# Kernel optimization log

Measured on AMD Instinct MI355X. Metric: run time of the kernel, lower is better.

The kernel has to match this reference:

```python
import jax, jax.numpy as jnp
import numpy as np

B, S, D, E, N, K = 4, 2048, 1024, 2048, 16, 4

def setup_inputs() -> dict:
    key = jax.random.key(0)
    ks = jax.random.split(key, 16)
    w = lambda k, shape, s=0.02: jax.random.normal(k, shape, dtype=jnp.float32) * s
    return {
        "x": jax.random.normal(ks[0], (B, S, D), dtype=jnp.float32),
        "ln_g": jnp.ones((D,), jnp.float32),
        "ln_b": jnp.zeros((D,), jnp.float32),
        "W_in": w(ks[1], (2 * E, D)),
        "b_in": jnp.zeros((2 * E,), jnp.float32),
        "conv_w": w(ks[2], (E, 1, K), 0.1),
        "conv_b": jnp.zeros((E,), jnp.float32),
        "A": w(ks[3], (E, N), 0.1),
        "Bm": w(ks[4], (E, N), 0.1),
        "W_c": w(ks[5], (E, E)),
        "b_c": jnp.zeros((E,), jnp.float32),
        "W_d": w(ks[6], (E, E)),
        "b_d": jnp.zeros((E,), jnp.float32),
        "log_delta": jnp.zeros((E,), jnp.float32),
        "W_out": w(ks[7], (D, E)),
        "b_out": jnp.zeros((D,), jnp.float32),
    }

def _layernorm(x, g, b, eps=1e-5):
    mu = jnp.mean(x, axis=-1, keepdims=True)
    var = jnp.var(x, axis=-1, keepdims=True)
    return (x - mu) * jax.lax.rsqrt(var + eps) * g + b

def _forward(x, ln_g, ln_b, W_in, b_in, conv_w, conv_b, A, Bm, W_c, b_c, W_d, b_d, log_delta, W_out, b_out):
    x_ln = _layernorm(x, ln_g, ln_b)
    x_proj = jnp.einsum("bsd,ed->bse", x_ln, W_in) + b_in  # (B,S,2E)
    xp, gate = jnp.split(x_proj, 2, axis=-1)
    # causal depthwise conv1d (torch pads K-1 both sides then truncates -> left pad only)
    xc = jax.lax.conv_general_dilated(
        xp.transpose(0, 2, 1), conv_w, (1,), [(K - 1, 0)],
        dimension_numbers=("NCH", "OIH", "NCH"), feature_group_count=E)
    xc = (xc + conv_b[None, :, None]).transpose(0, 2, 1)  # (B,S,E)
    xc = jax.nn.silu(xc)
    # selective SSM
    delta = jax.nn.softplus(log_delta)
    A_diag = jnp.exp(-delta)  # (E,)
    u = (jnp.einsum("bse,fe->bsf", xc, W_c) + b_c) * jax.nn.sigmoid(jnp.einsum("bse,fe->bsf", xc, W_d) + b_d)
    def step(h, u_t):
        # h: (B,E,N), u_t: (B,E)
        h = h * A_diag[None, :, None] + u_t[:, :, None] * Bm[None]
        y = jnp.sum(h * A[None], axis=-1)  # (B,E)
        return h, y
    h0 = jnp.zeros((x.shape[0], E, N), x.dtype)
    _, ys = jax.lax.scan(step, h0, u.transpose(1, 0, 2))  # ys: (S,B,E)
    x_ssm = ys.transpose(1, 0, 2)
    x_gated = x_ssm * jax.nn.sigmoid(gate)
    out = jnp.einsum("bse,de->bsd", x_gated, W_out) + b_out
    return out + x

def reference(x, ln_g, ln_b, W_in, b_in, conv_w, conv_b, A, Bm, W_c, b_c, W_d, b_d, log_delta, W_out, b_out):
    return _forward(x, ln_g, ln_b, W_in, b_in, conv_w, conv_b, A, Bm, W_c, b_c, W_d, b_d, log_delta, W_out, b_out)
```

## Files before the change

### kernel.cpp

```cpp
#include <hip/hip_runtime.h>
#include <hip/hip_bf16.h>

typedef __bf16 bf16_t;
typedef unsigned char u8;
typedef __bf16 bf16x8 __attribute__((ext_vector_type(8)));
typedef __bf16 bf16x4 __attribute__((ext_vector_type(4)));
typedef float  f32x4  __attribute__((ext_vector_type(4)));
typedef int    i32x4  __attribute__((ext_vector_type(4)));
typedef int    i32x8  __attribute__((ext_vector_type(8)));
typedef __attribute__((address_space(3))) unsigned as3u32;
typedef __attribute__((address_space(1))) unsigned as1u32;

#define Bdim 4
#define Sdim 2048
#define Ddim 1024
#define Edim 2048
#define CH 64
#define CL 32

#define WSCALE 32.0f
#define XCSCALE 16.0f
#define GSCALE 256.0f

__device__ __forceinline__ void gload_lds16(const void* g, void* l) {
  __builtin_amdgcn_global_load_lds((const as1u32*)g, (as3u32*)l, 16, 0, 0);
}
__device__ __forceinline__ float sigmoidf_(float x) {
  return 1.f / (1.f + __expf(-x));
}
__device__ __forceinline__ int pk_fp8x4(float a, float b, float c, float d) {
  int p = __builtin_amdgcn_cvt_pk_fp8_f32(a, b, 0, 0);
  p = __builtin_amdgcn_cvt_pk_fp8_f32(c, d, p, 1);
  return p;
}

__global__ __launch_bounds__(256)
void cvt_fp8_3(const float* __restrict__ s0, const float* __restrict__ s1,
               const float* __restrict__ s2, u8* __restrict__ d0,
               u8* __restrict__ d1, u8* __restrict__ d2) {
  const int seg = blockIdx.x >> 12;
  const int i   = ((blockIdx.x & 4095) * 256 + threadIdx.x) * 4;
  const float* s = (seg == 0) ? s0 : (seg == 1) ? s1 : s2;
  u8*          d = (seg == 0) ? d0 : (seg == 1) ? d1 : d2;
  *(int*)(d + i) = pk_fp8x4(s[i] * WSCALE, s[i + 1] * WSCALE,
                            s[i + 2] * WSCALE, s[i + 3] * WSCALE);
}

__global__ __launch_bounds__(256)
void cvt_fp8(const float* __restrict__ s, u8* __restrict__ d, int n, float scale) {
  int i = (blockIdx.x * 256 + threadIdx.x) * 4;
  if (i < n)
    *(int*)(d + i) = pk_fp8x4(s[i] * scale, s[i + 1] * scale,
                              s[i + 2] * scale, s[i + 3] * scale);
}

__global__ __launch_bounds__(256)
void prep_scalars(const float* __restrict__ ld, const float* __restrict__ Am,
                  const float* __restrict__ Bm, float* __restrict__ aexp,
                  float* __restrict__ Ce) {
  int e = blockIdx.x * 256 + threadIdx.x;
  if (e >= Edim) return;
  float d = ld[e];
  float sp = (d > 20.f) ? d : log1pf(expf(d));
  aexp[e] = expf(-sp);
  float s = 0.f;
  #pragma unroll
  for (int n = 0; n < 16; ++n) s += Am[e * 16 + n] * Bm[e * 16 + n];
  Ce[e] = s;
}

__global__ __launch_bounds__(256)
void ln_kernel(const float* __restrict__ x, const float* __restrict__ g,
               const float* __restrict__ b, u8* __restrict__ out) {
  const int row = blockIdx.x;
  const int tid = threadIdx.x;
  const float4 v = ((const float4*)(x + (size_t)row * Ddim))[tid];
  float s  = v.x + v.y + v.z + v.w;
  float ss = v.x * v.x + v.y * v.y + v.z * v.z + v.w * v.w;
  #pragma unroll
  for (int o = 32; o > 0; o >>= 1) { s += __shfl_down(s, o); ss += __shfl_down(ss, o); }
  __shared__ float sh[8];
  const int wv = tid >> 6, lane = tid & 63;
  if (lane == 0) { sh[wv] = s; sh[4 + wv] = ss; }
  __syncthreads();
  s  = sh[0] + sh[1] + sh[2] + sh[3];
  ss = sh[4] + sh[5] + sh[6] + sh[7];
  const float mean = s * (1.f / Ddim);
  const float var  = ss * (1.f / Ddim) - mean * mean;
  const float rstd = rsqrtf(var + 1e-5f);
  const float4 gv = ((const float4*)g)[tid];
  const float4 bv = ((const float4*)b)[tid];
  *(int*)(out + (size_t)row * Ddim + tid * 4) =
      pk_fp8x4((v.x - mean) * rstd * gv.x + bv.x,
               (v.y - mean) * rstd * gv.y + bv.y,
               (v.z - mean) * rstd * gv.z + bv.z,
               (v.w - mean) * rstd * gv.w + bv.w);
}

#define BM 128
#define BN 128

template<int MODE>
__global__ __launch_bounds__(256)
void gemm_mx(const u8* __restrict__ A, const u8* __restrict__ Bw,
             const float* __restrict__ bias, const bf16_t* __restrict__ X,
             const float* __restrict__ R, bf16_t* __restrict__ Cb,
             float* __restrict__ Cf, float descale, int M, int N, int K) {
  __shared__ __align__(16) u8 As[BM * 128];
  __shared__ __align__(16) u8 Bs[BN * 128];

  const int tid  = threadIdx.x;
  const int lane = tid & 63;
  const int wv   = tid >> 6;
  const int m0   = blockIdx.y * BM;
  const int n0   = blockIdx.x * BN;

  const int wr = (wv >> 1) * 64;
  const int wc = (wv & 1) * 64;
  const int tq = lane >> 4;
  const int tr = lane & 15;

  f32x4 acc[4][4] = {};

  size_t srcOff[4];
  int    ldsOff[4];
  #pragma unroll
  for (int g = 0; g < 4; ++g) {
    const int p   = g * 256 + tid;
    const int row = p >> 3;
    const int c   = (p & 7) ^ (row & 7);
    srcOff[g] = (size_t)row * K + c * 16;
    ldsOff[g] = g * 4096 + wv * 1024;
  }
  const size_t aBase = (size_t)m0 * K;
  const size_t bBase = (size_t)n0 * K;
  char* AsB = (char*)As;
  char* BsB = (char*)Bs;

  const int s7 = tr & 7;
  const int p0 = (((tq << 1)) ^ s7) * 16;
  const int p1 = (((tq << 1) | 1) ^ s7) * 16;

  for (int k0 = 0; k0 < K; k0 += 128) {
    __syncthreads();
    #pragma unroll
    for (int g = 0; g < 4; ++g)
      gload_lds16(A + aBase + srcOff[g] + k0, AsB + ldsOff[g]);
    #pragma unroll
    for (int g = 0; g < 4; ++g)
      gload_lds16(Bw + bBase + srcOff[g] + k0, BsB + ldsOff[g]);
    __syncthreads();

    i32x8 aF[4], bF[4];
    #pragma unroll
    for (int i = 0; i < 4; ++i) {
      const int rb = (wr + i * 16 + tr) * 128;
      const i32x4 lo = *(const i32x4*)&As[rb + p0];
      const i32x4 hi = *(const i32x4*)&As[rb + p1];
      aF[i] = __builtin_shufflevector(lo, hi, 0, 1, 2, 3, 4, 5, 6, 7);
    }
    #pragma unroll
    for (int j = 0; j < 4; ++j) {
      const int rb = (wc + j * 16 + tr) * 128;
      const i32x4 lo = *(const i32x4*)&Bs[rb + p0];
      const i32x4 hi = *(const i32x4*)&Bs[rb + p1];
      bF[j] = __builtin_shufflevector(lo, hi, 0, 1, 2, 3, 4, 5, 6, 7);
    }
    #pragma unroll
    for (int i = 0; i < 4; ++i)
      #pragma unroll
      for (int j = 0; j < 4; ++j)
        acc[i][j] = __builtin_amdgcn_mfma_scale_f32_16x16x128_f8f6f4(
            aF[i], bF[j], acc[i][j], 0, 0, 0, 0x7F, 0, 0x7F);
  }

  #pragma unroll
  for (int i = 0; i < 4; ++i) {
    #pragma unroll
    for (int j = 0; j < 4; ++j) {
      const int col = n0 + wc + j * 16 + tr;
      const float bv = bias[col];
      #pragma unroll
      for (int r = 0; r < 4; ++r) {
        const int rowg = m0 + wr + i * 16 + tq * 4 + r;
        const size_t idx = (size_t)rowg * N + col;
        const float v = acc[i][j][r] * descale + bv;
        if (MODE == 1)      Cf[idx] = v + R[idx];
        else if (MODE == 2) Cb[idx] = (bf16_t)((float)X[idx] * sigmoidf_(v));
        else                Cb[idx] = (bf16_t)v;
      }
    }
  }
}

__global__ __launch_bounds__(256)
void conv_silu(const bf16_t* __restrict__ xpg, const float* __restrict__ cw,
               const float* __restrict__ cb, u8* __restrict__ xc) {
  const int e  = blockIdx.y * 256 + threadIdx.x;
  const int b  = blockIdx.x >> 9;
  const int s0 = (blockIdx.x & 511) * 4;
  const float w0 = cw[e * 4 + 0], w1 = cw[e * 4 + 1], w2 = cw[e * 4 + 2], w3 = cw[e * 4 + 3];
  const float bias = cb[e];
  float xv[7];
  #pragma unroll
  for (int j = 0; j < 7; ++j) {
    const int s = s0 - 3 + j;
    xv[j] = (s >= 0) ? (float)xpg[(size_t)(b * Sdim + s) * (2 * Edim) + e] : 0.f;
  }
  #pragma unroll
  for (int t = 0; t < 4; ++t) {
    float a = fmaf(w0, xv[t], fmaf(w1, xv[t + 1], fmaf(w2, xv[t + 2], fmaf(w3, xv[t + 3], bias))));
    float y = a * sigmoidf_(a) * XCSCALE;
    int p = __builtin_amdgcn_cvt_pk_fp8_f32(y, y, 0, 0);
    xc[(size_t)(b * Sdim + s0 + t) * Edim + e] = (u8)(p & 0xff);
  }
}

__global__ __launch_bounds__(256)
void scan_part1(const bf16_t* __restrict__ u, const float* __restrict__ aexp,
                float* __restrict__ zloc) {
  const int c    = blockIdx.x;
  const int b    = blockIdx.y >> 3;
  const int eblk = blockIdx.y & 7;
  const int e    = eblk * 256 + threadIdx.x;
  const float a  = aexp[e];
  const bf16_t* up = u + ((size_t)(b * Sdim + c * CL)) * Edim + e;
  float z = 0.f;
  #pragma unroll
  for (int t = 0; t < CL; ++t) z = fmaf(a, z, (float)up[(size_t)t * Edim]);
  zloc[((size_t)b * CH + c) * Edim + e] = z;
}

__global__ __launch_bounds__(256)
void scan_part2(const float* __restrict__ aexp, float* __restrict__ zloc) {
  const int idx = blockIdx.x * 256 + threadIdx.x;
  const int b = idx >> 11, e = idx & (Edim - 1);
  float a  = aexp[e];
  float aL = a * a;
  aL = aL * aL; aL = aL * aL; aL = aL * aL; aL = aL * aL;
  float* zp = zloc + (size_t)b * CH * Edim + e;
  float pref = 0.f;
  #pragma unroll 4
  for (int c = 0; c < CH; ++c) {
    const float loc = zp[(size_t)c * Edim];
    zp[(size_t)c * Edim] = pref;
    pref = fmaf(aL, pref, loc);
  }
}

__global__ __launch_bounds__(256)
void scan_part3(const bf16_t* __restrict__ u, const bf16_t* __restrict__ xpg,
                const float* __restrict__ aexp, const float* __restrict__ Ce,
                const float* __restrict__ zloc, u8* __restrict__ xg8) {
  const int c    = blockIdx.x;
  const int b    = blockIdx.y >> 3;
  const int eblk = blockIdx.y & 7;
  const int e    = eblk * 256 + threadIdx.x;
  const float a = aexp[e], C = Ce[e];
  float z = zloc[((size_t)b * CH + c) * Edim + e];
  const bf16_t* up = u   + ((size_t)(b * Sdim + c * CL)) * Edim + e;
  const bf16_t* gp = xpg + ((size_t)(b * Sdim + c * CL)) * (2 * Edim) + Edim + e;
  u8*           op = xg8 + ((size_t)(b * Sdim + c * CL)) * Edim + e;
  #pragma unroll 8
  for (int t = 0; t < CL; ++t) {
    z = fmaf(a, z, (float)up[(size_t)t * Edim]);
    const float gv = (float)gp[(size_t)t * (2 * Edim)];
    const float y  = C * z * sigmoidf_(gv) * GSCALE;
    int p = __builtin_amdgcn_cvt_pk_fp8_f32(y, y, 0, 0);
    op[(size_t)t * Edim] = (u8)(p & 0xff);
  }
}

extern "C" void kernel_launch(void* const* d_in, const int* in_sizes, int n_in,
                              void* d_out, int out_size, void* d_ws, size_t ws_size,
                              hipStream_t stream) {
  const float* x         = (const float*)d_in[0];
  const float* ln_g      = (const float*)d_in[1];
  const float* ln_b      = (const float*)d_in[2];
  const float* W_in      = (const float*)d_in[3];
  const float* b_in      = (const float*)d_in[4];
  const float* conv_w    = (const float*)d_in[5];
  const float* conv_b    = (const float*)d_in[6];
  const float* Am        = (const float*)d_in[7];
  const float* Bm        = (const float*)d_in[8];
  const float* W_c       = (const float*)d_in[9];
  const float* b_c       = (const float*)d_in[10];
  const float* W_d       = (const float*)d_in[11];
  const float* b_d       = (const float*)d_in[12];
  const float* log_delta = (const float*)d_in[13];
  const float* W_out     = (const float*)d_in[14];
  const float* b_out     = (const float*)d_in[15];
  float* out = (float*)d_out;

  const size_t MiB = 1024 * 1024;
  char* w = (char*)d_ws;
  u8*     wWin8  = (u8*)    (w + 0);
  u8*     wWc8   = (u8*)    (w + 4 * MiB);
  u8*     wWd8   = (u8*)    (w + 8 * MiB);
  u8*     wWout8 = (u8*)    (w + 12 * MiB);
  float*  aexp   = (float*) (w + 15 * MiB);
  float*  Ce     = (float*) (w + 15 * MiB + 16384);
  float*  zloc   = (float*) (w + 15 * MiB + 65536);
  u8*     xln8   = (u8*)    (w + 18 * MiB);
  bf16_t* xpg    = (bf16_t*)(w + 26 * MiB);
  u8*     xc8    = (u8*)    (w + 90 * MiB);
  bf16_t* cbuf   = (bf16_t*)(w + 106 * MiB);
  bf16_t* ubuf   = (bf16_t*)(w + 138 * MiB);
  u8*     xg8    = (u8*)    (w + 170 * MiB);

  const int M = Bdim * Sdim;
  const float dsIn  = 1.f / WSCALE;
  const float dsCD  = 1.f / (WSCALE * XCSCALE);
  const float dsOut = 1.f / (WSCALE * GSCALE);

  cvt_fp8_3<<<3 * 4096, 256, 0, stream>>>(W_in, W_c, W_d, wWin8, wWc8, wWd8);
  cvt_fp8<<<(Ddim * Edim) / 1024, 256, 0, stream>>>(W_out, wWout8, Ddim * Edim, WSCALE);
  prep_scalars<<<Edim / 256, 256, 0, stream>>>(log_delta, Am, Bm, aexp, Ce);

  ln_kernel<<<M, 256, 0, stream>>>(x, ln_g, ln_b, xln8);

  gemm_mx<0><<<dim3((2 * Edim) / BN, M / BM), 256, 0, stream>>>(
      xln8, wWin8, b_in, nullptr, nullptr, xpg, nullptr, dsIn, M, 2 * Edim, Ddim);

  conv_silu<<<dim3(Bdim * (Sdim / 4), Edim / 256), 256, 0, stream>>>(xpg, conv_w, conv_b, xc8);

  gemm_mx<0><<<dim3(Edim / BN, M / BM), 256, 0, stream>>>(
      xc8, wWc8, b_c, nullptr, nullptr, cbuf, nullptr, dsCD, M, Edim, Edim);
  gemm_mx<2><<<dim3(Edim / BN, M / BM), 256, 0, stream>>>(
      xc8, wWd8, b_d, cbuf, nullptr, ubuf, nullptr, dsCD, M, Edim, Edim);

  scan_part1<<<dim3(CH, Bdim * (Edim / 256)), 256, 0, stream>>>(ubuf, aexp, zloc);
  scan_part2<<<(Bdim * Edim) / 256, 256, 0, stream>>>(aexp, zloc);
  scan_part3<<<dim3(CH, Bdim * (Edim / 256)), 256, 0, stream>>>(ubuf, xpg, aexp, Ce, zloc, xg8);

  gemm_mx<1><<<dim3(Ddim / BN, M / BM), 256, 0, stream>>>(
      xg8, wWout8, b_out, nullptr, x, nullptr, out, dsOut, M, Ddim, Edim);

  (void)in_sizes; (void)n_in; (void)out_size; (void)ws_size;
}
```

Before: 374.2 us.

## Store intermediate activations as scaled FP8 and vectorize conv/scan kernels

GEMM epilogues now write the input projection, the W_c output and the gated u tensor as scaled FP8 bytes instead of bf16. The conv, scan_part1 and scan_part3 kernels are rewritten so each thread handles four channels, using packed 4-byte FP8 loads and stores. This halves intermediate memory traffic and cuts the number of byte-wide accesses, at the cost of extra quantization error in the gate, xp, c and u values. That error feeds the recurrent scan and could hurt accuracy.

Measured after the change: 373.0 us. About the same (-0.3%).

```diff
diff --git a/kernel.cpp b/kernel.cpp
--- a/kernel.cpp
+++ b/kernel.cpp
@@ -3,8 +3,6 @@
 
 typedef __bf16 bf16_t;
 typedef unsigned char u8;
-typedef __bf16 bf16x8 __attribute__((ext_vector_type(8)));
-typedef __bf16 bf16x4 __attribute__((ext_vector_type(4)));
 typedef float  f32x4  __attribute__((ext_vector_type(4)));
 typedef int    i32x4  __attribute__((ext_vector_type(4)));
 typedef int    i32x8  __attribute__((ext_vector_type(8)));
@@ -19,7 +17,9 @@
 #define CL 32
 
 #define WSCALE 32.0f
+#define XPSCALE 32.0f
 #define XCSCALE 16.0f
+#define CSCALE 16.0f
 #define GSCALE 256.0f
 
 __device__ __forceinline__ void gload_lds16(const void* g, void* l) {
@@ -32,6 +32,13 @@
   int p = __builtin_amdgcn_cvt_pk_fp8_f32(a, b, 0, 0);
   p = __builtin_amdgcn_cvt_pk_fp8_f32(c, d, p, 1);
   return p;
+}
+template<int K>
+__device__ __forceinline__ float dq8(int v) {
+  return __builtin_amdgcn_cvt_f32_fp8(v, K);
+}
+__device__ __forceinline__ u8 q8(float v) {
+  return (u8)(__builtin_amdgcn_cvt_pk_fp8_f32(v, v, 0, 0) & 0xff);
 }
 
 __global__ __launch_bounds__(256)
@@ -103,9 +110,10 @@
 template<int MODE>
 __global__ __launch_bounds__(256)
 void gemm_mx(const u8* __restrict__ A, const u8* __restrict__ Bw,
-             const float* __restrict__ bias, const bf16_t* __restrict__ X,
-             const float* __restrict__ R, bf16_t* __restrict__ Cb,
-             float* __restrict__ Cf, float descale, int M, int N, int K) {
+             const float* __restrict__ bias, const u8* __restrict__ X,
+             const float* __restrict__ R, u8* __restrict__ C8,
+             float* __restrict__ Cf, float descale, float oscale,
+             int M, int N, int K) {
   __shared__ __align__(16) u8 As[BM * 128];
   __shared__ __align__(16) u8 Bs[BN * 128];
 
@@ -185,50 +193,76 @@
         const int rowg = m0 + wr + i * 16 + tq * 4 + r;
         const size_t idx = (size_t)rowg * N + col;
         const float v = acc[i][j][r] * descale + bv;
-        if (MODE == 1)      Cf[idx] = v + R[idx];
-        else if (MODE == 2) Cb[idx] = (bf16_t)((float)X[idx] * sigmoidf_(v));
-        else                Cb[idx] = (bf16_t)v;
+        if (MODE == 1) {
+          Cf[idx] = v + R[idx];
+        } else if (MODE == 2) {
+          const float xv = dq8<0>((int)X[idx]);
+          C8[idx] = q8(xv * sigmoidf_(v));
+        } else {
+          C8[idx] = q8(v * oscale);
+        }
       }
     }
   }
 }
 
 __global__ __launch_bounds__(256)
-void conv_silu(const bf16_t* __restrict__ xpg, const float* __restrict__ cw,
-               const float* __restrict__ cb, u8* __restrict__ xc) {
-  const int e  = blockIdx.y * 256 + threadIdx.x;
+void conv_silu(const u8* __restrict__ xpg8, const float* __restrict__ cw,
+               const float* __restrict__ cb, u8* __restrict__ xc8) {
+  const int e0 = (blockIdx.y * 256 + threadIdx.x) * 4;
   const int b  = blockIdx.x >> 9;
   const int s0 = (blockIdx.x & 511) * 4;
-  const float w0 = cw[e * 4 + 0], w1 = cw[e * 4 + 1], w2 = cw[e * 4 + 2], w3 = cw[e * 4 + 3];
-  const float bias = cb[e];
-  float xv[7];
+  float w[4][4], bias[4];
+  #pragma unroll
+  for (int k = 0; k < 4; ++k) {
+    const float4 wv = *(const float4*)(cw + (e0 + k) * 4);
+    w[k][0] = wv.x; w[k][1] = wv.y; w[k][2] = wv.z; w[k][3] = wv.w;
+    bias[k] = cb[e0 + k];
+  }
+  float f[7][4];
   #pragma unroll
   for (int j = 0; j < 7; ++j) {
     const int s = s0 - 3 + j;
-    xv[j] = (s >= 0) ? (float)xpg[(size_t)(b * Sdim + s) * (2 * Edim) + e] : 0.f;
+    const int xv = (s >= 0) ? *(const int*)(xpg8 + (size_t)(b * Sdim + s) * (2 * Edim) + e0) : 0;
+    f[j][0] = dq8<0>(xv); f[j][1] = dq8<1>(xv);
+    f[j][2] = dq8<2>(xv); f[j][3] = dq8<3>(xv);
   }
   #pragma unroll
   for (int t = 0; t < 4; ++t) {
-    float a = fmaf(w0, xv[t], fmaf(w1, xv[t + 1], fmaf(w2, xv[t + 2], fmaf(w3, xv[t + 3], bias))));
-    float y = a * sigmoidf_(a) * XCSCALE;
-    int p = __builtin_amdgcn_cvt_pk_fp8_f32(y, y, 0, 0);
-    xc[(size_t)(b * Sdim + s0 + t) * Edim + e] = (u8)(p & 0xff);
-  }
-}
-
-__global__ __launch_bounds__(256)
-void scan_part1(const bf16_t* __restrict__ u, const float* __restrict__ aexp,
+    float y[4];
+    #pragma unroll
+    for (int k = 0; k < 4; ++k) {
+      float a = fmaf(w[k][0], f[t][k],
+               fmaf(w[k][1], f[t + 1][k],
+               fmaf(w[k][2], f[t + 2][k],
+                    w[k][3] * f[t + 3][k])));
+      a = a * (1.f / XPSCALE) + bias[k];
+      y[k] = a * sigmoidf_(a) * XCSCALE;
+    }
+    *(int*)(xc8 + (size_t)(b * Sdim + s0 + t) * Edim + e0) =
+        pk_fp8x4(y[0], y[1], y[2], y[3]);
+  }
+}
+
+__global__ __launch_bounds__(256)
+void scan_part1(const u8* __restrict__ u8p, const float* __restrict__ aexp,
                 float* __restrict__ zloc) {
-  const int c    = blockIdx.x;
-  const int b    = blockIdx.y >> 3;
-  const int eblk = blockIdx.y & 7;
-  const int e    = eblk * 256 + threadIdx.x;
-  const float a  = aexp[e];
-  const bf16_t* up = u + ((size_t)(b * Sdim + c * CL)) * Edim + e;
-  float z = 0.f;
-  #pragma unroll
-  for (int t = 0; t < CL; ++t) z = fmaf(a, z, (float)up[(size_t)t * Edim]);
-  zloc[((size_t)b * CH + c) * Edim + e] = z;
+  const int c  = blockIdx.x;
+  const int b  = blockIdx.y >> 1;
+  const int e0 = ((blockIdx.y & 1) * 256 + threadIdx.x) * 4;
+  const float4 av = *(const float4*)(aexp + e0);
+  const u8* up = u8p + ((size_t)(b * Sdim + c * CL)) * Edim + e0;
+  float z0 = 0.f, z1 = 0.f, z2 = 0.f, z3 = 0.f;
+  #pragma unroll
+  for (int t = 0; t < CL; ++t) {
+    const int uv = *(const int*)(up + (size_t)t * Edim);
+    z0 = fmaf(av.x, z0, dq8<0>(uv));
+    z1 = fmaf(av.y, z1, dq8<1>(uv));
+    z2 = fmaf(av.z, z2, dq8<2>(uv));
+    z3 = fmaf(av.w, z3, dq8<3>(uv));
+  }
+  float4 zv = {z0, z1, z2, z3};
+  *(float4*)(zloc + ((size_t)b * CH + c) * Edim + e0) = zv;
 }
 
 __global__ __launch_bounds__(256)
@@ -249,25 +283,33 @@
 }
 
 __global__ __launch_bounds__(256)
-void scan_part3(const bf16_t* __restrict__ u, const bf16_t* __restrict__ xpg,
+void scan_part3(const u8* __restrict__ u8p, const u8* __restrict__ xpg8,
                 const float* __restrict__ aexp, const float* __restrict__ Ce,
                 const float* __restrict__ zloc, u8* __restrict__ xg8) {
-  const int c    = blockIdx.x;
-  const int b    = blockIdx.y >> 3;
-  const int eblk = blockIdx.y & 7;
-  const int e    = eblk * 256 + threadIdx.x;
-  const float a = aexp[e], C = Ce[e];
-  float z = zloc[((size_t)b * CH + c) * Edim + e];
-  const bf16_t* up = u   + ((size_t)(b * Sdim + c * CL)) * Edim + e;
-  const bf16_t* gp = xpg + ((size_t)(b * Sdim + c * CL)) * (2 * Edim) + Edim + e;
-  u8*           op = xg8 + ((size_t)(b * Sdim + c * CL)) * Edim + e;
-  #pragma unroll 8
+  const int c  = blockIdx.x;
+  const int b  = blockIdx.y >> 1;
+  const int e0 = ((blockIdx.y & 1) * 256 + threadIdx.x) * 4;
+  const float4 av = *(const float4*)(aexp + e0);
+  float4 Cv = *(const float4*)(Ce + e0);
+  const float cs = GSCALE / CSCALE;
+  Cv.x *= cs; Cv.y *= cs; Cv.z *= cs; Cv.w *= cs;
+  float4 zv = *(const float4*)(zloc + ((size_t)b * CH + c) * Edim + e0);
+  const u8* up = u8p  + ((size_t)(b * Sdim + c * CL)) * Edim + e0;
+  const u8* gp = xpg8 + ((size_t)(b * Sdim + c * CL)) * (2 * Edim) + Edim + e0;
+  u8*       op = xg8  + ((size_t)(b * Sdim + c * CL)) * Edim + e0;
+  #pragma unroll 4
   for (int t = 0; t < CL; ++t) {
-    z = fmaf(a, z, (float)up[(size_t)t * Edim]);
-    const float gv = (float)gp[(size_t)t * (2 * Edim)];
-    const float y  = C * z * sigmoidf_(gv) * GSCALE;
-    int p = __builtin_amdgcn_cvt_pk_fp8_f32(y, y, 0, 0);
-    op[(size_t)t * Edim] = (u8)(p & 0xff);
+    const int uv = *(const int*)(up + (size_t)t * Edim);
+    const int gv = *(const int*)(gp + (size_t)t * (2 * Edim));
+    zv.x = fmaf(av.x, zv.x, dq8<0>(uv));
+    zv.y = fmaf(av.y, zv.y, dq8<1>(uv));
+    zv.z = fmaf(av.z, zv.z, dq8<2>(uv));
+    zv.w = fmaf(av.w, zv.w, dq8<3>(uv));
+    const float y0 = Cv.x * zv.x * sigmoidf_(dq8<0>(gv) * (1.f / XPSCALE));
+    const float y1 = Cv.y * zv.y * sigmoidf_(dq8<1>(gv) * (1.f / XPSCALE));
+    const float y2 = Cv.z * zv.z * sigmoidf_(dq8<2>(gv) * (1.f / XPSCALE));
+    const float y3 = Cv.w * zv.w * sigmoidf_(dq8<3>(gv) * (1.f / XPSCALE));
+    *(int*)(op + (size_t)t * Edim) = pk_fp8x4(y0, y1, y2, y3);
   }
 }
 
@@ -294,19 +336,19 @@
 
   const size_t MiB = 1024 * 1024;
   char* w = (char*)d_ws;
-  u8*     wWin8  = (u8*)    (w + 0);
-  u8*     wWc8   = (u8*)    (w + 4 * MiB);
-  u8*     wWd8   = (u8*)    (w + 8 * MiB);
-  u8*     wWout8 = (u8*)    (w + 12 * MiB);
-  float*  aexp   = (float*) (w + 15 * MiB);
-  float*  Ce     = (float*) (w + 15 * MiB + 16384);
-  float*  zloc   = (float*) (w + 15 * MiB + 65536);
-  u8*     xln8   = (u8*)    (w + 18 * MiB);
-  bf16_t* xpg    = (bf16_t*)(w + 26 * MiB);
-  u8*     xc8    = (u8*)    (w + 90 * MiB);
-  bf16_t* cbuf   = (bf16_t*)(w + 106 * MiB);
-  bf16_t* ubuf   = (bf16_t*)(w + 138 * MiB);
-  u8*     xg8    = (u8*)    (w + 170 * MiB);
+  u8*     wWin8  = (u8*)   (w + 0);
+  u8*     wWc8   = (u8*)   (w + 4 * MiB);
+  u8*     wWd8   = (u8*)   (w + 8 * MiB);
+  u8*     wWout8 = (u8*)   (w + 12 * MiB);
+  float*  aexp   = (float*)(w + 15 * MiB);
+  float*  Ce     = (float*)(w + 15 * MiB + 16384);
+  float*  zloc   = (float*)(w + 15 * MiB + 65536);
+  u8*     xln8   = (u8*)   (w + 18 * MiB);
+  u8*     xpg8   = (u8*)   (w + 26 * MiB);
+  u8*     xc8    = (u8*)   (w + 58 * MiB);
+  u8*     c8     = (u8*)   (w + 74 * MiB);
+  u8*     u8b    = (u8*)   (w + 90 * MiB);
+  u8*     xg8    = (u8*)   (w + 106 * MiB);
 
   const int M = Bdim * Sdim;
   const float dsIn  = 1.f / WSCALE;
@@ -319,22 +361,22 @@
 
   ln_kernel<<<M, 256, 0, stream>>>(x, ln_g, ln_b, xln8);
 
-  gemm_mx<0><<<dim3((2 * Edim) / BN, M / BM), 256, 0, stream>>>(
-      xln8, wWin8, b_in, nullptr, nullptr, xpg, nullptr, dsIn, M, 2 * Edim, Ddim);
-
-  conv_silu<<<dim3(Bdim * (Sdim / 4), Edim / 256), 256, 0, stream>>>(xpg, conv_w, conv_b, xc8);
-
-  gemm_mx<0><<<dim3(Edim / BN, M / BM), 256, 0, stream>>>(
-      xc8, wWc8, b_c, nullptr, nullptr, cbuf, nullptr, dsCD, M, Edim, Edim);
+  gemm_mx<3><<<dim3((2 * Edim) / BN, M / BM), 256, 0, stream>>>(
+      xln8, wWin8, b_in, nullptr, nullptr, xpg8, nullptr, dsIn, XPSCALE, M, 2 * Edim, Ddim);
+
+  conv_silu<<<dim3(Bdim * (Sdim / 4), Edim / 1024), 256, 0, stream>>>(xpg8, conv_w, conv_b, xc8);
+
+  gemm_mx<3><<<dim3(Edim / BN, M / BM), 256, 0, stream>>>(
+      xc8, wWc8, b_c, nullptr, nullptr, c8, nullptr, dsCD, CSCALE, M, Edim, Edim);
   gemm_mx<2><<<dim3(Edim / BN, M / BM), 256, 0, stream>>>(
-      xc8, wWd8, b_d, cbuf, nullptr, ubuf, nullptr, dsCD, M, Edim, Edim);
-
-  scan_part1<<<dim3(CH, Bdim * (Edim / 256)), 256, 0, stream>>>(ubuf, aexp, zloc);
+      xc8, wWd8, b_d, c8, nullptr, u8b, nullptr, dsCD, 1.f, M, Edim, Edim);
+
+  scan_part1<<<dim3(CH, Bdim * 2), 256, 0, stream>>>(u8b, aexp, zloc);
   scan_part2<<<(Bdim * Edim) / 256, 256, 0, stream>>>(aexp, zloc);
-  scan_part3<<<dim3(CH, Bdim * (Edim / 256)), 256, 0, stream>>>(ubuf, xpg, aexp, Ce, zloc, xg8);
+  scan_part3<<<dim3(CH, Bdim * 2), 256, 0, stream>>>(u8b, xpg8, aexp, Ce, zloc, xg8);
 
   gemm_mx<1><<<dim3(Ddim / BN, M / BM), 256, 0, stream>>>(
-      xg8, wWout8, b_out, nullptr, x, nullptr, out, dsOut, M, Ddim, Edim);
+      xg8, wWout8, b_out, nullptr, x, nullptr, out, dsOut, 1.f, M, Ddim, Edim);
 
   (void)in_sizes; (void)n_in; (void)out_size; (void)ws_size;
 }
```
